# Performance work log

Measured on AMD Instinct MI355X. Metric: run time of the kernel, lower is better.

## Reference

```python
import jax, jax.numpy as jnp
import numpy as np

D, K, HID, NBLK, N = 128, 256, 256, 2, 4096

def setup_inputs() -> dict:
    key = jax.random.key(0)
    ks = jax.random.split(key, 12)
    inp = {
        'x': jax.random.normal(ks[0], (N, D), jnp.float32),
        'x_hat': jax.random.normal(ks[1], (N, D), jnp.float32),
        'base_codebook': jax.random.normal(ks[2], (K, D), jnp.float32) * 0.1,
        # concat_proj: Linear(2D -> D), torch weight layout (out, in)
        'Wp': jax.random.normal(ks[3], (D, 2 * D), jnp.float32) / np.sqrt(2 * D),
        'bp': jnp.zeros((D,), jnp.float32),
        # residual blocks stacked over NBLK: Linear(D->HID), ReLU, Linear(HID->D)
        'W1': jax.random.normal(ks[4], (NBLK, HID, D), jnp.float32) / np.sqrt(D),
        'b1': jnp.zeros((NBLK, HID), jnp.float32),
        'W2': jax.random.normal(ks[5], (NBLK, D, HID), jnp.float32) / np.sqrt(HID),
        'b2': jnp.zeros((NBLK, D), jnp.float32),
    }
    return inp

def _forward(x, x_hat, base_codebook, Wp, bp, W1, b1, W2, b2):
    # concat_proj([x_hat, cbar]) decomposed: avoids materializing (N,K,2D)
    x_part = x_hat @ Wp[:, :D].T                      # (N, D)
    c_part = base_codebook @ Wp[:, D:].T + bp          # (K, D)
    C = x_part[:, None, :] + c_part[None, :, :]        # (N, K, D)
    for i in range(NBLK):
        h = jax.nn.relu(jnp.einsum('nkd,hd->nkh', C, W1[i]) + b1[i])
        C = C + jnp.einsum('nkh,dh->nkd', h, W2[i]) + b2[i]
    r = x - x_hat                                      # (N, D)
    dists = jnp.sum((r[:, None, :] - C) ** 2, axis=-1) # (N, K)
    codes = jnp.argmin(dists, axis=-1)                 # (N,)
    c_sel = jnp.take_along_axis(C, codes[:, None, None], axis=1)[:, 0, :]
    x_hat_new = x_hat + c_sel
    return codes, x_hat_new, r, c_sel

def reference(x, x_hat, base_codebook, Wp, bp, W1, b1, W2, b2):
    return _forward(x, x_hat, base_codebook, Wp, bp, W1, b1, W2, b2)
```

## Files before the change

kernel.cpp:

```cpp
#include <hip/hip_runtime.h>


#define QD    128
#define QK    256
#define QHID  256
#define QNBLK 2
#define QN    4096

typedef _Float16 f16;
typedef _Float16 f16x8  __attribute__((ext_vector_type(8)));
typedef float    f32x16 __attribute__((ext_vector_type(16)));
typedef unsigned u32x2  __attribute__((ext_vector_type(2)));

#define WS_CPART 0
#define WS_W1H   131072
#define WS_W1L   262144
#define WS_W2H   393216
#define WS_W2L   524288

static __device__ __forceinline__ f32x16 MF32(f16x8 a, f16x8 b, f32x16 c) {
    return __builtin_amdgcn_mfma_f32_32x32x16_f16(a, b, c, 0, 0, 0);
}
static __device__ __forceinline__ unsigned pkrtz(float a, float b) {
    return __builtin_bit_cast(unsigned, __builtin_amdgcn_cvt_pkrtz(a, b));
}
static __device__ __forceinline__ float f32lo(unsigned p) {
    return (float)__builtin_bit_cast(f16, (unsigned short)(p & 0xffffu));
}
static __device__ __forceinline__ float f32hi(unsigned p) {
    return (float)__builtin_bit_cast(f16, (unsigned short)(p >> 16));
}
static __device__ __forceinline__ u32x2 plswap(unsigned a, unsigned b) {
    return __builtin_amdgcn_permlane32_swap(a, b, false, false);
}

template<int RB>
static __device__ __forceinline__ void split_frags(f32x16 a, f16x8& fh, f16x8& fl) {
    unsigned P0 = pkrtz(a[RB + 0], a[RB + 1]);
    unsigned P1 = pkrtz(a[RB + 2], a[RB + 3]);
    unsigned Q0 = pkrtz(a[RB + 4], a[RB + 5]);
    unsigned Q1 = pkrtz(a[RB + 6], a[RB + 7]);
    unsigned L0 = pkrtz(a[RB + 0] - f32lo(P0), a[RB + 1] - f32hi(P0));
    unsigned L1 = pkrtz(a[RB + 2] - f32lo(P1), a[RB + 3] - f32hi(P1));
    unsigned L2 = pkrtz(a[RB + 4] - f32lo(Q0), a[RB + 5] - f32hi(Q0));
    unsigned L3 = pkrtz(a[RB + 6] - f32lo(Q1), a[RB + 7] - f32hi(Q1));
    u32x2 s0 = plswap(P0, Q0);
    u32x2 s1 = plswap(P1, Q1);
    u32x2 t0 = plswap(L0, L2);
    u32x2 t1 = plswap(L1, L3);
    uint4 hw = make_uint4(s0.x, s1.x, s0.y, s1.y);
    uint4 lw = make_uint4(t0.x, t1.x, t0.y, t1.y);
    fh = __builtin_bit_cast(f16x8, hw);
    fl = __builtin_bit_cast(f16x8, lw);
}

__global__ __launch_bounds__(128) void qinco_prep(
    const float* __restrict__ cb, const float* __restrict__ Wp,
    const float* __restrict__ bp, const float* __restrict__ W1,
    const float* __restrict__ W2, char* __restrict__ ws) {
    const int blk = blockIdx.x;
    const int t = threadIdx.x;
    __shared__ float row[QD];

    if (blk < 256) {
        float* cpart = (float*)(ws + WS_CPART);
        row[t] = cb[blk * QD + t];
        __syncthreads();
        float acc = bp[t];
        const float* wr = Wp + (size_t)t * (2 * QD) + QD;
        #pragma unroll 8
        for (int e = 0; e < QD; ++e) acc = fmaf(row[e], wr[e], acc);
        cpart[blk * QD + t] = acc;
    } else if (blk < 384) {
        if (t < 64) {
            const int cid = blk - 256;
            const int b = cid >> 6, hc = (cid >> 3) & 7, kc = cid & 7;
            const int m = t & 31, g = t >> 5;
            f16* w1h = (f16*)(ws + WS_W1H);
            f16* w1l = (f16*)(ws + WS_W1L);
            #pragma unroll
            for (int j = 0; j < 8; ++j) {
                float wv = W1[((size_t)b * QHID + hc * 32 + m) * QD + kc * 16 + g * 8 + j];
                f16 hi = (f16)wv;
                size_t idx = ((size_t)cid * 64 + t) * 8 + j;
                w1h[idx] = hi;
                w1l[idx] = (f16)(wv - (float)hi);
            }
        }
    } else {
        if (t < 64) {
            const int e = blk - 384;
            const int b = e >> 6, hc = (e >> 3) & 7, dt = (e >> 1) & 3, kch = e & 1;
            const int m = t & 31, g = t >> 5;
            f16* w2h = (f16*)(ws + WS_W2H);
            f16* w2l = (f16*)(ws + WS_W2L);
            #pragma unroll
            for (int j = 0; j < 8; ++j) {
                float wv = W2[((size_t)b * QD + dt * 32 + m) * QHID + hc * 32 + kch * 16 + g * 8 + j];
                f16 hi = (f16)wv;
                size_t idx = ((size_t)e * 64 + t) * 8 + j;
                w2h[idx] = hi;
                w2l[idx] = (f16)(wv - (float)hi);
            }
        }
    }
}

__global__ __launch_bounds__(512, 2) void qinco_main(
    const float* __restrict__ x, const float* __restrict__ xh,
    const float* __restrict__ Wp,
    const float* __restrict__ b1g, const float* __restrict__ b2g,
    const char* __restrict__ ws, float* __restrict__ out) {

    __shared__ float b1_s[2 * QHID];
    __shared__ float b2_s[2 * QD];
    __shared__ float red_d[QK];
    __shared__ int   red_i[QK];
    __shared__ float xp_s[QD], xh_s[QD], r_s[QD], csel[QD];

    const int n = blockIdx.x;
    const int t = threadIdx.x;
    const int w = t >> 6;
    const int l = t & 63;
    const int c32 = l & 31;
    const int g = l >> 5;
    const int baserow = w * 32;

    const float* cpart = (const float*)(ws + WS_CPART);

    b1_s[t] = b1g[t];
    if (t < 2 * QD) b2_s[t] = b2g[t];
    if (t < QD) {
        float xv  = x[(size_t)n * QD + t];
        float xhv = xh[(size_t)n * QD + t];
        xh_s[t] = xhv;
        r_s[t]  = xv - xhv;
    }
    __syncthreads();

    if (t < QD) {
        const float4* wr = (const float4*)(Wp + (size_t)t * (2 * QD));
        const float4* xv = (const float4*)xh_s;
        float acc = 0.f;
        #pragma unroll
        for (int j = 0; j < QD / 4; ++j) {
            float4 a = wr[j], bv = xv[j];
            acc = fmaf(a.x, bv.x, acc);
            acc = fmaf(a.y, bv.y, acc);
            acc = fmaf(a.z, bv.z, acc);
            acc = fmaf(a.w, bv.w, acc);
        }
        xp_s[t] = acc;
    }
    __syncthreads();

    f32x16 Cacc[4];
    {
        const float* cprow = cpart + (size_t)(baserow + c32) * QD;
        #pragma unroll
        for (int dt = 0; dt < 4; ++dt)
            #pragma unroll
            for (int rq = 0; rq < 4; ++rq) {
                const int off = dt * 32 + 8 * rq + 4 * g;
                float4 cp  = *(const float4*)(cprow + off);
                float4 xp4 = *(const float4*)(xp_s + off);
                Cacc[dt][rq * 4 + 0] = cp.x + xp4.x;
                Cacc[dt][rq * 4 + 1] = cp.y + xp4.y;
                Cacc[dt][rq * 4 + 2] = cp.z + xp4.z;
                Cacc[dt][rq * 4 + 3] = cp.w + xp4.w;
            }
    }

    #pragma unroll 1
    for (int b = 0; b < QNBLK; ++b) {
        const char* pw1h = ws + WS_W1H + (size_t)b * 65536 + (size_t)l * 16;
        const char* pw1l = ws + WS_W1L + (size_t)b * 65536 + (size_t)l * 16;
        const char* pw2h = ws + WS_W2H + (size_t)b * 65536 + (size_t)l * 16;
        const char* pw2l = ws + WS_W2L + (size_t)b * 65536 + (size_t)l * 16;

        f16x8 cfh[8], cfl[8];
        #pragma unroll
        for (int dt = 0; dt < 4; ++dt) {
            split_frags<0>(Cacc[dt], cfh[dt * 2 + 0], cfl[dt * 2 + 0]);
            split_frags<8>(Cacc[dt], cfh[dt * 2 + 1], cfl[dt * 2 + 1]);
        }

        #pragma unroll
        for (int hc = 0; hc < 8; ++hc) {
            f32x16 Ha, Hb, Hc;
            #pragma unroll
            for (int rq = 0; rq < 4; ++rq) {
                float4 bv = *(const float4*)(b1_s + b * QHID + hc * 32 + 8 * rq + 4 * g);
                Ha[rq * 4 + 0] = bv.x;
                Ha[rq * 4 + 1] = bv.y;
                Ha[rq * 4 + 2] = bv.z;
                Ha[rq * 4 + 3] = bv.w;
            }
            #pragma unroll
            for (int r = 0; r < 16; ++r) { Hb[r] = 0.f; Hc[r] = 0.f; }
            #pragma unroll
            for (int kc = 0; kc < 8; ++kc) {
                f16x8 wh = *(const f16x8*)(pw1h + (size_t)(hc * 8 + kc) * 1024);
                f16x8 wl = *(const f16x8*)(pw1l + (size_t)(hc * 8 + kc) * 1024);
                Ha = MF32(wh, cfh[kc], Ha);
                Hb = MF32(wl, cfh[kc], Hb);
                Hc = MF32(wh, cfl[kc], Hc);
            }
            f32x16 H;
            #pragma unroll
            for (int r = 0; r < 16; ++r)
                H[r] = fmaxf(Ha[r] + Hb[r] + Hc[r], 0.f);

            f16x8 hfh0, hfl0, hfh1, hfl1;
            split_frags<0>(H, hfh0, hfl0);
            split_frags<8>(H, hfh1, hfl1);

            #pragma unroll
            for (int dt = 0; dt < 4; ++dt) {
                const char* q2h = pw2h + (size_t)(hc * 8 + dt * 2) * 1024;
                const char* q2l = pw2l + (size_t)(hc * 8 + dt * 2) * 1024;
                f16x8 w2h0 = *(const f16x8*)(q2h);
                f16x8 w2l0 = *(const f16x8*)(q2l);
                f16x8 w2h1 = *(const f16x8*)(q2h + 1024);
                f16x8 w2l1 = *(const f16x8*)(q2l + 1024);
                Cacc[dt] = MF32(w2h0, hfh0, Cacc[dt]);
                Cacc[dt] = MF32(w2l0, hfh0, Cacc[dt]);
                Cacc[dt] = MF32(w2h0, hfl0, Cacc[dt]);
                Cacc[dt] = MF32(w2h1, hfh1, Cacc[dt]);
                Cacc[dt] = MF32(w2l1, hfh1, Cacc[dt]);
                Cacc[dt] = MF32(w2h1, hfl1, Cacc[dt]);
            }
        }

        #pragma unroll
        for (int dt = 0; dt < 4; ++dt)
            #pragma unroll
            for (int rq = 0; rq < 4; ++rq) {
                float4 bv = *(const float4*)(b2_s + b * QD + dt * 32 + 8 * rq + 4 * g);
                Cacc[dt][rq * 4 + 0] += bv.x;
                Cacc[dt][rq * 4 + 1] += bv.y;
                Cacc[dt][rq * 4 + 2] += bv.z;
                Cacc[dt][rq * 4 + 3] += bv.w;
            }
    }

    float pa = 0.f, pb = 0.f, pc = 0.f, pdm = 0.f;
    #pragma unroll
    for (int dt = 0; dt < 4; ++dt)
        #pragma unroll
        for (int rq = 0; rq < 4; ++rq) {
            float4 rr = *(const float4*)(r_s + dt * 32 + 8 * rq + 4 * g);
            float t0 = rr.x - Cacc[dt][rq * 4 + 0];
            float t1 = rr.y - Cacc[dt][rq * 4 + 1];
            float t2 = rr.z - Cacc[dt][rq * 4 + 2];
            float t3 = rr.w - Cacc[dt][rq * 4 + 3];
            pa = fmaf(t0, t0, pa);
            pb = fmaf(t1, t1, pb);
            pc = fmaf(t2, t2, pc);
            pdm = fmaf(t3, t3, pdm);
        }
    float pd = (pa + pb) + (pc + pdm);
    pd += __shfl_xor(pd, 32);
    if (l < 32) {
        red_d[baserow + l] = pd;
        red_i[baserow + l] = baserow + l;
    }
    __syncthreads();

    for (int off = 128; off > 0; off >>= 1) {
        if (t < off) {
            float d2 = red_d[t + off]; int i2 = red_i[t + off];
            float d1 = red_d[t];       int i1 = red_i[t];
            if (d2 < d1 || (d2 == d1 && i2 < i1)) { red_d[t] = d2; red_i[t] = i2; }
        }
        __syncthreads();
    }
    const int code = red_i[0];

    if (w == (code >> 5) && c32 == (code & 31)) {
        #pragma unroll
        for (int dt = 0; dt < 4; ++dt)
            #pragma unroll
            for (int rq = 0; rq < 4; ++rq)
                *(float4*)(csel + dt * 32 + 8 * rq + 4 * g) =
                    make_float4(Cacc[dt][rq * 4 + 0], Cacc[dt][rq * 4 + 1],
                                Cacc[dt][rq * 4 + 2], Cacc[dt][rq * 4 + 3]);
    }
    __syncthreads();

    if (t == 0) out[n] = (float)code;
    if (t < QD) {
        float cs  = csel[t];
        out[QN + (size_t)n * QD + t]                       = xh_s[t] + cs;
        out[QN + (size_t)QN * QD + (size_t)n * QD + t]     = r_s[t];
        out[QN + 2 * (size_t)QN * QD + (size_t)n * QD + t] = cs;
    }
}

extern "C" void kernel_launch(void* const* d_in, const int* in_sizes, int n_in,
                              void* d_out, int out_size, void* d_ws, size_t ws_size,
                              hipStream_t stream) {
    const float* x   = (const float*)d_in[0];
    const float* xh  = (const float*)d_in[1];
    const float* cb  = (const float*)d_in[2];
    const float* Wp  = (const float*)d_in[3];
    const float* bp  = (const float*)d_in[4];
    const float* W1  = (const float*)d_in[5];
    const float* b1  = (const float*)d_in[6];
    const float* W2  = (const float*)d_in[7];
    const float* b2  = (const float*)d_in[8];
    float* out = (float*)d_out;

    qinco_prep<<<512, 128, 0, stream>>>(cb, Wp, bp, W1, W2, (char*)d_ws);
    qinco_main<<<QN, 512, 0, stream>>>(x, xh, Wp, b1, b2, (const char*)d_ws, out);
}
```

Baseline: 861.4 us.

## Stage weight tiles through double-buffered LDS with async global-to-LDS loads

```diff
diff --git a/kernel.cpp b/kernel.cpp
--- a/kernel.cpp
+++ b/kernel.cpp
@@ -18,6 +18,17 @@
 #define WS_W2H   393216
 #define WS_W2L   524288
 
+#define L_WBUF  0
+#define L_B1    65536
+#define L_B2    67584
+#define L_REDD  68608
+#define L_REDI  69632
+#define L_XP    70656
+#define L_XH    71168
+#define L_RS    71680
+#define L_CSEL  72192
+#define L_TOTAL 72704
+
 static __device__ __forceinline__ f32x16 MF32(f16x8 a, f16x8 b, f32x16 c) {
     return __builtin_amdgcn_mfma_f32_32x32x16_f16(a, b, c, 0, 0, 0);
 }
@@ -32,6 +43,11 @@
 }
 static __device__ __forceinline__ u32x2 plswap(unsigned a, unsigned b) {
     return __builtin_amdgcn_permlane32_swap(a, b, false, false);
+}
+static __device__ __forceinline__ void gload_lds16(const void* g, void* l) {
+    __builtin_amdgcn_global_load_lds(
+        (const __attribute__((address_space(1))) unsigned*)g,
+        (__attribute__((address_space(3))) unsigned*)l, 16, 0, 0);
 }
 
 template<int RB>
@@ -112,12 +128,7 @@
     const float* __restrict__ b1g, const float* __restrict__ b2g,
     const char* __restrict__ ws, float* __restrict__ out) {
 
-    __shared__ float b1_s[2 * QHID];
-    __shared__ float b2_s[2 * QD];
-    __shared__ float red_d[QK];
-    __shared__ int   red_i[QK];
-    __shared__ float xp_s[QD], xh_s[QD], r_s[QD], csel[QD];
-
+    extern __shared__ char smem[];
     const int n = blockIdx.x;
     const int t = threadIdx.x;
     const int w = t >> 6;
@@ -125,6 +136,17 @@
     const int c32 = l & 31;
     const int g = l >> 5;
     const int baserow = w * 32;
+    const int plane = w >> 1;
+    const int jbase = (w & 1) * 4;
+
+    float* b1_s  = (float*)(smem + L_B1);
+    float* b2_s  = (float*)(smem + L_B2);
+    float* red_d = (float*)(smem + L_REDD);
+    int*   red_i = (int*)(smem + L_REDI);
+    float* xp_s  = (float*)(smem + L_XP);
+    float* xh_s  = (float*)(smem + L_XH);
+    float* r_s   = (float*)(smem + L_RS);
+    float* csel  = (float*)(smem + L_CSEL);
 
     const float* cpart = (const float*)(ws + WS_CPART);
 
@@ -171,77 +193,111 @@
             }
     }
 
+    {
+        const char* s0 = ws + (size_t)(plane + 1) * 131072 + (size_t)jbase * 1024
+                       + (size_t)l * 16;
+        char* d0 = smem + L_WBUF + (size_t)(plane * 8 + jbase) * 1024;
+        #pragma unroll
+        for (int ii = 0; ii < 4; ++ii)
+            gload_lds16(s0 + (size_t)ii * 1024, d0 + (size_t)ii * 1024);
+    }
+
+    f16x8 cfh[8], cfl[8];
+
     #pragma unroll 1
-    for (int b = 0; b < QNBLK; ++b) {
-        const char* pw1h = ws + WS_W1H + (size_t)b * 65536 + (size_t)l * 16;
-        const char* pw1l = ws + WS_W1L + (size_t)b * 65536 + (size_t)l * 16;
-        const char* pw2h = ws + WS_W2H + (size_t)b * 65536 + (size_t)l * 16;
-        const char* pw2l = ws + WS_W2L + (size_t)b * 65536 + (size_t)l * 16;
-
-        f16x8 cfh[8], cfl[8];
+    for (int iter = 0; iter < 16; ++iter) {
+        const int cur = iter & 1;
+        const int b = iter >> 3;
+        const int hc = iter & 7;
+
+        asm volatile("s_waitcnt vmcnt(0)" ::: "memory");
+        __syncthreads();
+
+        if (iter < 15) {
+            const int it2 = iter + 1;
+            const int bb = it2 >> 3, hh = it2 & 7;
+            const char* s0 = ws + (size_t)(plane + 1) * 131072 + (size_t)bb * 65536
+                           + (size_t)(hh * 8 + jbase) * 1024 + (size_t)l * 16;
+            char* d0 = smem + L_WBUF + (size_t)(cur ^ 1) * 32768
+                     + (size_t)(plane * 8 + jbase) * 1024;
+            #pragma unroll
+            for (int ii = 0; ii < 4; ++ii)
+                gload_lds16(s0 + (size_t)ii * 1024, d0 + (size_t)ii * 1024);
+        }
+
+        if (hc == 0) {
+            #pragma unroll
+            for (int dt = 0; dt < 4; ++dt) {
+                split_frags<0>(Cacc[dt], cfh[dt * 2 + 0], cfl[dt * 2 + 0]);
+                split_frags<8>(Cacc[dt], cfh[dt * 2 + 1], cfl[dt * 2 + 1]);
+            }
+        }
+
+        const char* wb = (const char*)smem + L_WBUF + (size_t)cur * 32768
+                       + (size_t)l * 16;
+
+        f32x16 Ha, Hb, Hc;
+        #pragma unroll
+        for (int rq = 0; rq < 4; ++rq) {
+            float4 bv = *(const float4*)(b1_s + b * QHID + hc * 32 + 8 * rq + 4 * g);
+            Ha[rq * 4 + 0] = bv.x;
+            Ha[rq * 4 + 1] = bv.y;
+            Ha[rq * 4 + 2] = bv.z;
+            Ha[rq * 4 + 3] = bv.w;
+        }
+        #pragma unroll
+        for (int r = 0; r < 16; ++r) { Hb[r] = 0.f; Hc[r] = 0.f; }
+
+        __builtin_amdgcn_s_setprio(1);
+        #pragma unroll
+        for (int kc = 0; kc < 8; ++kc) {
+            f16x8 wh = *(const f16x8*)(wb + kc * 1024);
+            f16x8 wl = *(const f16x8*)(wb + 8192 + kc * 1024);
+            Ha = MF32(wh, cfh[kc], Ha);
+            Hb = MF32(wl, cfh[kc], Hb);
+            Hc = MF32(wh, cfl[kc], Hc);
+        }
+        __builtin_amdgcn_s_setprio(0);
+
+        f32x16 H;
+        #pragma unroll
+        for (int r = 0; r < 16; ++r)
+            H[r] = fmaxf(Ha[r] + Hb[r] + Hc[r], 0.f);
+
+        f16x8 hfh0, hfl0, hfh1, hfl1;
+        split_frags<0>(H, hfh0, hfl0);
+        split_frags<8>(H, hfh1, hfl1);
+
+        __builtin_amdgcn_s_setprio(1);
         #pragma unroll
         for (int dt = 0; dt < 4; ++dt) {
-            split_frags<0>(Cacc[dt], cfh[dt * 2 + 0], cfl[dt * 2 + 0]);
-            split_frags<8>(Cacc[dt], cfh[dt * 2 + 1], cfl[dt * 2 + 1]);
-        }
-
-        #pragma unroll
-        for (int hc = 0; hc < 8; ++hc) {
-            f32x16 Ha, Hb, Hc;
-            #pragma unroll
-            for (int rq = 0; rq < 4; ++rq) {
-                float4 bv = *(const float4*)(b1_s + b * QHID + hc * 32 + 8 * rq + 4 * g);
-                Ha[rq * 4 + 0] = bv.x;
-                Ha[rq * 4 + 1] = bv.y;
-                Ha[rq * 4 + 2] = bv.z;
-                Ha[rq * 4 + 3] = bv.w;
-            }
-            #pragma unroll
-            for (int r = 0; r < 16; ++r) { Hb[r] = 0.f; Hc[r] = 0.f; }
-            #pragma unroll
-            for (int kc = 0; kc < 8; ++kc) {
-                f16x8 wh = *(const f16x8*)(pw1h + (size_t)(hc * 8 + kc) * 1024);
-                f16x8 wl = *(const f16x8*)(pw1l + (size_t)(hc * 8 + kc) * 1024);
-                Ha = MF32(wh, cfh[kc], Ha);
-                Hb = MF32(wl, cfh[kc], Hb);
-                Hc = MF32(wh, cfl[kc], Hc);
-            }
-            f32x16 H;
-            #pragma unroll
-            for (int r = 0; r < 16; ++r)
-                H[r] = fmaxf(Ha[r] + Hb[r] + Hc[r], 0.f);
-
-            f16x8 hfh0, hfl0, hfh1, hfl1;
-            split_frags<0>(H, hfh0, hfl0);
-            split_frags<8>(H, hfh1, hfl1);
-
-            #pragma unroll
-            for (int dt = 0; dt < 4; ++dt) {
-                const char* q2h = pw2h + (size_t)(hc * 8 + dt * 2) * 1024;
-                const char* q2l = pw2l + (size_t)(hc * 8 + dt * 2) * 1024;
-                f16x8 w2h0 = *(const f16x8*)(q2h);
-                f16x8 w2l0 = *(const f16x8*)(q2l);
-                f16x8 w2h1 = *(const f16x8*)(q2h + 1024);
-                f16x8 w2l1 = *(const f16x8*)(q2l + 1024);
-                Cacc[dt] = MF32(w2h0, hfh0, Cacc[dt]);
-                Cacc[dt] = MF32(w2l0, hfh0, Cacc[dt]);
-                Cacc[dt] = MF32(w2h0, hfl0, Cacc[dt]);
-                Cacc[dt] = MF32(w2h1, hfh1, Cacc[dt]);
-                Cacc[dt] = MF32(w2l1, hfh1, Cacc[dt]);
-                Cacc[dt] = MF32(w2h1, hfl1, Cacc[dt]);
-            }
-        }
-
-        #pragma unroll
-        for (int dt = 0; dt < 4; ++dt)
-            #pragma unroll
-            for (int rq = 0; rq < 4; ++rq) {
-                float4 bv = *(const float4*)(b2_s + b * QD + dt * 32 + 8 * rq + 4 * g);
-                Cacc[dt][rq * 4 + 0] += bv.x;
-                Cacc[dt][rq * 4 + 1] += bv.y;
-                Cacc[dt][rq * 4 + 2] += bv.z;
-                Cacc[dt][rq * 4 + 3] += bv.w;
-            }
+            const char* q2h = wb + 16384 + (size_t)(dt * 2) * 1024;
+            const char* q2l = wb + 24576 + (size_t)(dt * 2) * 1024;
+            f16x8 w2h0 = *(const f16x8*)(q2h);
+            f16x8 w2l0 = *(const f16x8*)(q2l);
+            f16x8 w2h1 = *(const f16x8*)(q2h + 1024);
+            f16x8 w2l1 = *(const f16x8*)(q2l + 1024);
+            Cacc[dt] = MF32(w2h0, hfh0, Cacc[dt]);
+            Cacc[dt] = MF32(w2l0, hfh0, Cacc[dt]);
+            Cacc[dt] = MF32(w2h0, hfl0, Cacc[dt]);
+            Cacc[dt] = MF32(w2h1, hfh1, Cacc[dt]);
+            Cacc[dt] = MF32(w2l1, hfh1, Cacc[dt]);
+            Cacc[dt] = MF32(w2h1, hfl1, Cacc[dt]);
+        }
+        __builtin_amdgcn_s_setprio(0);
+
+        if (hc == 7) {
+            #pragma unroll
+            for (int dt = 0; dt < 4; ++dt)
+                #pragma unroll
+                for (int rq = 0; rq < 4; ++rq) {
+                    float4 bv = *(const float4*)(b2_s + b * QD + dt * 32 + 8 * rq + 4 * g);
+                    Cacc[dt][rq * 4 + 0] += bv.x;
+                    Cacc[dt][rq * 4 + 1] += bv.y;
+                    Cacc[dt][rq * 4 + 2] += bv.z;
+                    Cacc[dt][rq * 4 + 3] += bv.w;
+                }
+        }
     }
 
     float pa = 0.f, pb = 0.f, pc = 0.f, pdm = 0.f;
@@ -312,5 +368,9 @@
     float* out = (float*)d_out;
 
     qinco_prep<<<512, 128, 0, stream>>>(cb, Wp, bp, W1, W2, (char*)d_ws);
-    qinco_main<<<QN, 512, 0, stream>>>(x, xh, Wp, b1, b2, (const char*)d_ws, out);
-}
+
+    (void)hipFuncSetAttribute((const void*)qinco_main,
+                              hipFuncAttributeMaxDynamicSharedMemorySize, L_TOTAL);
+    qinco_main<<<QN, 512, L_TOTAL, stream>>>(x, xh, Wp, b1, b2,
+                                             (const char*)d_ws, out);
+}
```

Result: faster. 716.0 us (-16.9%).
